# Optimization experiments

Measured on AMD Instinct MI355X. Metric: run time of the kernel, lower is better.

## Reference

```python
import jax, jax.numpy as jnp
import numpy as np

# Layered type graph: L layers of M nodes; layer 0 = basic types, layers >=1 reference earlier layers only.
L, M, D, P, S = 64, 2048, 128, 4, 2
NB = 11  # number of Kotlin basic types (kotlin.Any ... kotlin.Unit)
N = L * M


def setup_inputs() -> dict:
    key = jax.random.key(0)
    ks = jax.random.split(key, 8)
    rng = np.random.default_rng(0)
    basic_names = jnp.asarray(rng.integers(0, NB, size=(M,)), dtype=jnp.int32)
    # properties / superTypes point strictly to earlier layers (valid topological DAG)
    prop_ids = np.zeros((L, M, P), dtype=np.int32)
    super_ids = np.zeros((L, M, S), dtype=np.int32)
    for l in range(1, L):
        prop_ids[l] = rng.integers(0, l * M, size=(M, P))
        super_ids[l] = rng.integers(0, l * M, size=(M, S))
    prop_ids = jnp.asarray(prop_ids)
    super_ids = jnp.asarray(super_ids)
    sc = 0.05
    return {
        "basic_names": basic_names,
        "prop_ids": prop_ids,
        "super_ids": super_ids,
        "basic_table": jax.random.normal(ks[0], (NB, D), jnp.float32) * sc,
        "W_m": jax.random.normal(ks[1], (D, 4 * D), jnp.float32) * sc,
        "U_m": jax.random.normal(ks[2], (D, 4 * D), jnp.float32) * sc,
        "b_m": jnp.zeros((4 * D,), jnp.float32),
        "W_s": jax.random.normal(ks[3], (D, 4 * D), jnp.float32) * sc,
        "U_s": jax.random.normal(ks[4], (D, 4 * D), jnp.float32) * sc,
        "b_s": jnp.zeros((4 * D,), jnp.float32),
        "empty_members": jax.random.normal(ks[5], (D,), jnp.float32) * sc,
    }


def _lstm_last(seq, W, U, b):
    # seq: [T, B, D]; keras LSTM (tanh / sigmoid, gate order i,f,g,o); returns last hidden [B, D]
    T, B, Dh = seq.shape
    h = jnp.zeros((B, Dh), seq.dtype)
    c = jnp.zeros((B, Dh), seq.dtype)
    for t in range(T):  # T is a small static constant (P+1 or S+1)
        z = seq[t] @ W + h @ U + b  # [B, 4D]
        i, f, g, o = jnp.split(z, 4, axis=-1)
        c = jax.nn.sigmoid(f) * c + jax.nn.sigmoid(i) * jnp.tanh(g)
        h = jax.nn.sigmoid(o) * jnp.tanh(c)
    return h


def reference(basic_names, prop_ids, super_ids, basic_table, W_m, U_m, b_m, W_s, U_s, b_s, empty_members):
    emb = jnp.zeros((N, D), basic_table.dtype)
    emb = emb.at[:M].set(basic_table[basic_names])  # layer 0: basic type embedding lookup

    def step(emb, xs):
        l, pid, sid = xs  # pid:[M,P] sid:[M,S], all indices < l*M (already computed)
        prop_e = jnp.swapaxes(emb[pid], 0, 1)  # [P, M, D] irregular gather
        seq_m = jnp.concatenate([jnp.broadcast_to(empty_members, (1, M, D)), prop_e], axis=0)  # [P+1, M, D]
        h_m = _lstm_last(seq_m, W_m, U_m, b_m)  # embed_members
        sup_e = jnp.swapaxes(emb[sid], 0, 1)  # [S, M, D]
        seq_s = jnp.concatenate([sup_e, h_m[None]], axis=0)  # [S+1, M, D]
        h_s = _lstm_last(seq_s, W_s, U_s, b_s)  # embed_super_types
        emb = jax.lax.dynamic_update_slice(emb, h_s, (l * M, 0))
        return emb, None

    ls = jnp.arange(1, L, dtype=jnp.int32)
    emb, _ = jax.lax.scan(step, emb, (ls, prop_ids[1:], super_ids[1:]))
    return emb  # [N, D] == tf.convert_to_tensor(class_embeddings)
```

## Files before the change

### kernel.cpp

```cpp
#include <hip/hip_runtime.h>

typedef unsigned short u16;
typedef short s16x8 __attribute__((ext_vector_type(8)));
typedef float f32x4 __attribute__((ext_vector_type(4)));

#define LAYERS   64
#define M_NODES  2048
#define DIM      128
#define FD       512
#define CHUNK    16
#define NBLK     128
#define TPB      512
#define XPAD     136

__device__ __forceinline__ u16 f2bf(float f) {
    union { float f; unsigned int i; } v; v.f = f;
    unsigned int r = (v.i + 0x7FFFu + ((v.i >> 16) & 1u)) >> 16;
    return (u16)r;
}
__device__ __forceinline__ float sigm(float x) {
    return __builtin_amdgcn_rcpf(1.0f + __builtin_exp2f(-1.44269504f * x));
}
__device__ __forceinline__ float tanh_f(float x) {
    float ax = __builtin_fabsf(x);
    float t  = __builtin_exp2f(-2.88539008f * ax);
    float r  = (1.0f - t) * __builtin_amdgcn_rcpf(1.0f + t);
    return __builtin_copysignf(r, x);
}

__global__ void l0_kernel(const int* __restrict__ names, const float* __restrict__ table,
                          float* __restrict__ emb) {
    int v = blockIdx.x * blockDim.x + threadIdx.x;
    if (v >= M_NODES * (DIM / 4)) return;
    int row = v >> 5, c = v & 31;
    const float4* src = (const float4*)(table + (size_t)names[row] * DIM);
    ((float4*)(emb + (size_t)row * DIM))[c] = src[c];
}

__global__ void repack_kernel(const float* __restrict__ Wm, const float* __restrict__ Um,
                              const float* __restrict__ Ws, const float* __restrict__ Us,
                              u16* __restrict__ packed) {
    int t = blockIdx.x * blockDim.x + threadIdx.x;
    if (t >= 4 * 4 * 32 * 64) return;
    int lane = t & 63, ntg = (t >> 6) & 31, kc = (t >> 11) & 3, mat = t >> 13;
    const float* B = (mat == 0) ? Wm : (mat == 1) ? Um : (mat == 2) ? Ws : Us;
    int q = lane >> 4, nl = lane & 15;
    int kb = kc * 32 + q * 8;
    int n  = ntg * 16 + nl;
    u16* dst = packed + ((((size_t)mat * 4 + kc) * 32 + ntg) * 64 + lane) * 8;
    #pragma unroll
    for (int j = 0; j < 8; j++) dst[j] = f2bf(B[(size_t)(kb + j) * FD + n]);
}

template <bool PACKED>
__global__ __launch_bounds__(TPB, 2) void layer_kernel(
    float* __restrict__ emb, const int* __restrict__ prop_ids, const int* __restrict__ super_ids,
    const float* __restrict__ Wm, const float* __restrict__ Um, const float* __restrict__ bm,
    const float* __restrict__ Ws, const float* __restrict__ Us, const float* __restrict__ bs,
    const float* __restrict__ empty, const u16* __restrict__ packed, int l) {

    __shared__ __align__(16) u16  xs[6][CHUNK][XPAD];
    __shared__ __align__(16) u16  hbuf[2][CHUNK][XPAD];
    __shared__ __align__(16) u16  empty_s[XPAD];

    const int tid  = threadIdx.x;
    const int b    = blockIdx.x;
    const int g0   = b * CHUNK;
    const size_t row0 = (size_t)l * M_NODES + g0;

    const int wv   = tid >> 6;
    const int lane = tid & 63;
    const int q    = lane >> 4, nl = lane & 15;
    const int d    = wv * 16 + nl;

    if (tid < 384) {
        int quarter = tid & 3;
        int r    = tid >> 2;
        int slot = r >> 4;
        int node = r & 15;
        size_t idx;
        if (slot < 4) idx = (size_t)prop_ids [((size_t)l * M_NODES + g0 + node) * 4 + slot];
        else          idx = (size_t)super_ids[((size_t)l * M_NODES + g0 + node) * 2 + (slot - 4)];
        const float4* src = (const float4*)(emb + idx * DIM);
        u16* dst = &xs[slot][node][0];
        int e0 = quarter * 32;
        #pragma unroll
        for (int j = 0; j < 8; j++) {
            float4 v = src[(e0 >> 2) + j];
            int o = e0 + j * 4;
            dst[o] = f2bf(v.x); dst[o + 1] = f2bf(v.y);
            dst[o + 2] = f2bf(v.z); dst[o + 3] = f2bf(v.w);
        }
    } else if (tid < 384 + 128) {
        int dd = tid - 384;
        empty_s[dd] = f2bf(empty[dd]);
    }
    __syncthreads();

    auto load_bfrag_packed = [&](int mat, int kc, int g) -> s16x8 {
        return *(const s16x8*)(packed + ((((size_t)mat * 4 + kc) * 32 + (g * 8 + wv)) * 64 + lane) * 8);
    };
    auto load_bfrag_direct = [&](const float* B, int kc, int g) -> s16x8 {
        int kb = kc * 32 + q * 8;
        int n  = g * 128 + d;
        s16x8 f;
        #pragma unroll
        for (int j = 0; j < 8; j++) f[j] = (short)f2bf(B[(size_t)(kb + j) * FD + n]);
        return f;
    };
    auto load_afrag = [&](const u16* X , int kc) -> s16x8 {
        return *(const s16x8*)(X + (size_t)nl * XPAD + kc * 32 + q * 8);
    };

    auto run_phase = [&](const float* Wg, const float* Ug, const float* bias,
                         int matW, int matU, int nsteps, const int* slots,
                         bool write_hm, bool write_out) {
        s16x8 wf[4][4], uf[4][4];
        #pragma unroll
        for (int kc = 0; kc < 4; kc++) {
            #pragma unroll
            for (int g = 0; g < 4; g++) {
                if (PACKED) { wf[kc][g] = load_bfrag_packed(matW, kc, g);
                              uf[kc][g] = load_bfrag_packed(matU, kc, g); }
                else        { wf[kc][g] = load_bfrag_direct(Wg, kc, g);
                              uf[kc][g] = load_bfrag_direct(Ug, kc, g); }
            }
        }
        float bz[4];
        #pragma unroll
        for (int g = 0; g < 4; g++) bz[g] = bias[g * 128 + d];
        float cc[4] = {0.f, 0.f, 0.f, 0.f};

        #pragma unroll 1
        for (int t = 0; t < nsteps; t++) {
            int s = slots[t];
            f32x4 acc[4];
            #pragma unroll
            for (int g = 0; g < 4; g++) acc[g] = (f32x4){0.f, 0.f, 0.f, 0.f};
            #pragma unroll
            for (int kc = 0; kc < 4; kc++) {
                s16x8 a = (s < 0) ? *(const s16x8*)(&empty_s[kc * 32 + q * 8])
                                  : load_afrag(&xs[s][0][0], kc);
                #pragma unroll
                for (int g = 0; g < 4; g++)
                    acc[g] = __builtin_amdgcn_mfma_f32_16x16x32_bf16(a, wf[kc][g], acc[g], 0, 0, 0);
            }
            if (t > 0) {
                __syncthreads();
                const u16* hb = &hbuf[(t - 1) & 1][0][0];
                #pragma unroll
                for (int kc = 0; kc < 4; kc++) {
                    s16x8 a = load_afrag(hb, kc);
                    #pragma unroll
                    for (int g = 0; g < 4; g++)
                        acc[g] = __builtin_amdgcn_mfma_f32_16x16x32_bf16(a, uf[kc][g], acc[g], 0, 0, 0);
                }
            }
            bool last = (t == nsteps - 1);
            #pragma unroll
            for (int r2 = 0; r2 < 4; r2++) {
                int m = q * 4 + r2;
                float zi = acc[0][r2] + bz[0];
                float zf = acc[1][r2] + bz[1];
                float zg = acc[2][r2] + bz[2];
                float zo = acc[3][r2] + bz[3];
                float c  = sigm(zf) * cc[r2] + sigm(zi) * tanh_f(zg);
                cc[r2] = c;
                float h  = sigm(zo) * tanh_f(c);
                if (!last)          hbuf[t & 1][m][d] = f2bf(h);
                else if (write_hm)  xs[0][m][d] = f2bf(h);
                else if (write_out) emb[(row0 + m) * DIM + d] = h;
            }
        }
    };

    {
        const int slots_m[5] = {-1, 0, 1, 2, 3};
        run_phase(Wm, Um, bm, 0, 1, 5, slots_m, true, false);
    }
    {
        const int slots_s[3] = {4, 5, 0};
        run_phase(Ws, Us, bs, 2, 3, 3, slots_s, false, true);
    }
}

extern "C" void kernel_launch(void* const* d_in, const int* in_sizes, int n_in,
                              void* d_out, int out_size, void* d_ws, size_t ws_size,
                              hipStream_t stream) {
    const int*   names = (const int*)d_in[0];
    const int*   pids  = (const int*)d_in[1];
    const int*   sids  = (const int*)d_in[2];
    const float* table = (const float*)d_in[3];
    const float* Wm    = (const float*)d_in[4];
    const float* Um    = (const float*)d_in[5];
    const float* bm    = (const float*)d_in[6];
    const float* Ws    = (const float*)d_in[7];
    const float* Us    = (const float*)d_in[8];
    const float* bs    = (const float*)d_in[9];
    const float* empt  = (const float*)d_in[10];
    float* emb  = (float*)d_out;
    u16* packed = (u16*)d_ws;

    l0_kernel<<<256, 256, 0, stream>>>(names, table, emb);

    const size_t packed_bytes = (size_t)4 * 4 * 32 * 64 * 8 * sizeof(u16);
    if (ws_size >= packed_bytes) {
        repack_kernel<<<128, 256, 0, stream>>>(Wm, Um, Ws, Us, packed);
        for (int l = 1; l < LAYERS; l++)
            layer_kernel<true><<<NBLK, TPB, 0, stream>>>(emb, pids, sids, Wm, Um, bm,
                                                         Ws, Us, bs, empt, packed, l);
    } else {
        for (int l = 1; l < LAYERS; l++)
            layer_kernel<false><<<NBLK, TPB, 0, stream>>>(emb, pids, sids, Wm, Um, bm,
                                                          Ws, Us, bs, empt, packed, l);
    }
}
```

Before: 1.269 ms.

## Fuse all layers into one cooperative persistent kernel with grid sync

```diff
diff --git a/kernel.cpp b/kernel.cpp
--- a/kernel.cpp
+++ b/kernel.cpp
@@ -1,4 +1,7 @@
 #include <hip/hip_runtime.h>
+#include <hip/hip_cooperative_groups.h>
+
+namespace cg = cooperative_groups;
 
 typedef unsigned short u16;
 typedef short s16x8 __attribute__((ext_vector_type(8)));
@@ -53,6 +56,241 @@
 }
 
 template <bool PACKED>
+__global__ __launch_bounds__(TPB, 2) void fused_kernel(
+    float* __restrict__ emb, const int* __restrict__ prop_ids, const int* __restrict__ super_ids,
+    const float* __restrict__ Wm, const float* __restrict__ Um, const float* __restrict__ bm,
+    const float* __restrict__ Ws, const float* __restrict__ Us, const float* __restrict__ bs,
+    const float* __restrict__ empty, const u16* __restrict__ packed) {
+
+    cg::grid_group grid = cg::this_grid();
+
+    __shared__ __align__(16) u16  xs[6][CHUNK][XPAD];
+    __shared__ __align__(16) u16  hbuf[2][CHUNK][XPAD];
+    __shared__ float h1_s[DIM];
+
+    const int tid  = threadIdx.x;
+    const int b    = blockIdx.x;
+    const int g0   = b * CHUNK;
+    const int wv   = tid >> 6;
+    const int lane = tid & 63;
+    const int q    = lane >> 4, nl = lane & 15;
+    const int d    = wv * 16 + nl;
+
+    auto ldB = [&](const float* B, int mat, int kc, int g) -> s16x8 {
+        if (PACKED) {
+            return *(const s16x8*)(packed + ((((size_t)mat * 4 + kc) * 32 + (g * 8 + wv)) * 64 + lane) * 8);
+        } else {
+            int kb = kc * 32 + q * 8;
+            int n  = g * 128 + d;
+            s16x8 f;
+            #pragma unroll
+            for (int j = 0; j < 8; j++) f[j] = (short)f2bf(B[(size_t)(kb + j) * FD + n]);
+            return f;
+        }
+    };
+    auto load_afrag = [&](const u16* X , int kc) -> s16x8 {
+        return *(const s16x8*)(X + (size_t)nl * XPAD + kc * 32 + q * 8);
+    };
+
+    float bzm[4], bzs[4];
+    #pragma unroll
+    for (int g = 0; g < 4; g++) { bzm[g] = bm[g * 128 + d]; bzs[g] = bs[g * 128 + d]; }
+
+    float c1, h1;
+    {
+        float z0 = bzm[0], z1 = bzm[1], z2 = bzm[2], z3 = bzm[3];
+        for (int k = 0; k < DIM; k++) {
+            float e = empty[k];
+            const float* Wr = Wm + (size_t)k * FD + d;
+            z0 += e * Wr[0]; z1 += e * Wr[128]; z2 += e * Wr[256]; z3 += e * Wr[384];
+        }
+        (void)z1;
+        c1 = sigm(z0) * tanh_f(z2);
+        h1 = sigm(z3) * tanh_f(c1);
+        if (q == 0) h1_s[d] = h1;
+    }
+    __syncthreads();
+
+    float uh1[4];
+    {
+        s16x8 ha[4];
+        #pragma unroll
+        for (int kc = 0; kc < 4; kc++)
+            #pragma unroll
+            for (int j = 0; j < 8; j++) ha[kc][j] = (short)f2bf(h1_s[kc * 32 + q * 8 + j]);
+        f32x4 acc[4];
+        #pragma unroll
+        for (int g = 0; g < 4; g++) acc[g] = (f32x4){0.f, 0.f, 0.f, 0.f};
+        #pragma unroll
+        for (int kc = 0; kc < 4; kc++) {
+            #pragma unroll
+            for (int g = 0; g < 4; g++) {
+                s16x8 u = ldB(Um, 1, kc, g);
+                acc[g] = __builtin_amdgcn_mfma_f32_16x16x32_bf16(ha[kc], u, acc[g], 0, 0, 0);
+            }
+        }
+        #pragma unroll
+        for (int g = 0; g < 4; g++) uh1[g] = acc[g][0];
+    }
+
+    auto gates = [&](f32x4* acc, const float* bz, float* cc, int mode, int parity, int l) {
+        #pragma unroll
+        for (int r2 = 0; r2 < 4; r2++) {
+            int m = q * 4 + r2;
+            float zi = acc[0][r2] + bz[0];
+            float zf = acc[1][r2] + bz[1];
+            float zg = acc[2][r2] + bz[2];
+            float zo = acc[3][r2] + bz[3];
+            float c  = sigm(zf) * cc[r2] + sigm(zi) * tanh_f(zg);
+            cc[r2] = c;
+            float h  = sigm(zo) * tanh_f(c);
+            if (mode == 0)      hbuf[parity][m][d] = f2bf(h);
+            else if (mode == 1) xs[0][m][d] = f2bf(h);
+            else emb[((size_t)l * M_NODES + g0 + m) * DIM + d] = h;
+        }
+    };
+
+    for (int l = 1; l < LAYERS; l++) {
+        size_t gidx = 0; int quarter = 0, slot = 0, node = 0;
+        if (tid < 384) {
+            quarter = tid & 3;
+            int r = tid >> 2;
+            slot = r >> 4;
+            node = r & 15;
+            if (slot < 4) gidx = (size_t)prop_ids [((size_t)l * M_NODES + g0 + node) * 4 + slot];
+            else          gidx = (size_t)super_ids[((size_t)l * M_NODES + g0 + node) * 2 + (slot - 4)];
+        }
+        if (l > 1) { __threadfence(); grid.sync(); }
+
+        if (tid < 384) {
+            const float4* src = (const float4*)(emb + gidx * DIM);
+            u16* dst = &xs[slot][node][0];
+            int e0 = quarter * 32;
+            #pragma unroll
+            for (int j = 0; j < 8; j++) {
+                float4 v = src[(e0 >> 2) + j];
+                int o = e0 + j * 4;
+                dst[o] = f2bf(v.x); dst[o + 1] = f2bf(v.y);
+                dst[o + 2] = f2bf(v.z); dst[o + 3] = f2bf(v.w);
+            }
+        }
+        __syncthreads();
+
+        f32x4 zxm[4][4];
+        {
+            s16x8 wf[4][4];
+            #pragma unroll
+            for (int kc = 0; kc < 4; kc++)
+                #pragma unroll
+                for (int g = 0; g < 4; g++) wf[kc][g] = ldB(Wm, 0, kc, g);
+            #pragma unroll
+            for (int s = 0; s < 4; s++) {
+                #pragma unroll
+                for (int g = 0; g < 4; g++) zxm[s][g] = (f32x4){0.f, 0.f, 0.f, 0.f};
+                #pragma unroll
+                for (int kc = 0; kc < 4; kc++) {
+                    s16x8 a = load_afrag(&xs[s][0][0], kc);
+                    #pragma unroll
+                    for (int g = 0; g < 4; g++)
+                        zxm[s][g] = __builtin_amdgcn_mfma_f32_16x16x32_bf16(a, wf[kc][g], zxm[s][g], 0, 0, 0);
+                }
+            }
+        }
+
+        {
+            s16x8 uf[4][4];
+            #pragma unroll
+            for (int kc = 0; kc < 4; kc++)
+                #pragma unroll
+                for (int g = 0; g < 4; g++) uf[kc][g] = ldB(Um, 1, kc, g);
+            float cc[4] = {c1, c1, c1, c1};
+            {
+                f32x4 acc[4];
+                #pragma unroll
+                for (int g = 0; g < 4; g++) acc[g] = zxm[0][g] + uh1[g];
+                gates(acc, bzm, cc, 0, 1, l);
+            }
+            #pragma unroll
+            for (int t = 2; t <= 4; t++) {
+                __syncthreads();
+                const u16* hb = &hbuf[(t - 1) & 1][0][0];
+                f32x4 acc[4];
+                #pragma unroll
+                for (int g = 0; g < 4; g++) acc[g] = zxm[t - 1][g];
+                #pragma unroll
+                for (int kc = 0; kc < 4; kc++) {
+                    s16x8 a = load_afrag(hb, kc);
+                    #pragma unroll
+                    for (int g = 0; g < 4; g++)
+                        acc[g] = __builtin_amdgcn_mfma_f32_16x16x32_bf16(a, uf[kc][g], acc[g], 0, 0, 0);
+                }
+                if (t < 4) gates(acc, bzm, cc, 0, t & 1, l);
+                else       gates(acc, bzm, cc, 1, 0, l);
+            }
+        }
+
+        {
+            s16x8 uf[4][4], wf[4][4];
+            #pragma unroll
+            for (int kc = 0; kc < 4; kc++)
+                #pragma unroll
+                for (int g = 0; g < 4; g++) {
+                    uf[kc][g] = ldB(Us, 3, kc, g);
+                    wf[kc][g] = ldB(Ws, 2, kc, g);
+                }
+            f32x4 acc0[4], zxs1[4];
+            #pragma unroll
+            for (int g = 0; g < 4; g++) { acc0[g] = (f32x4){0.f,0.f,0.f,0.f}; zxs1[g] = (f32x4){0.f,0.f,0.f,0.f}; }
+            #pragma unroll
+            for (int kc = 0; kc < 4; kc++) {
+                s16x8 a4 = load_afrag(&xs[4][0][0], kc);
+                s16x8 a5 = load_afrag(&xs[5][0][0], kc);
+                #pragma unroll
+                for (int g = 0; g < 4; g++) {
+                    acc0[g] = __builtin_amdgcn_mfma_f32_16x16x32_bf16(a4, wf[kc][g], acc0[g], 0, 0, 0);
+                    zxs1[g] = __builtin_amdgcn_mfma_f32_16x16x32_bf16(a5, wf[kc][g], zxs1[g], 0, 0, 0);
+                }
+            }
+            float cc[4] = {0.f, 0.f, 0.f, 0.f};
+            gates(acc0, bzs, cc, 0, 0, l);
+            {
+                __syncthreads();
+                const u16* hb = &hbuf[0][0][0];
+                f32x4 acc[4];
+                #pragma unroll
+                for (int g = 0; g < 4; g++) acc[g] = zxs1[g];
+                #pragma unroll
+                for (int kc = 0; kc < 4; kc++) {
+                    s16x8 a = load_afrag(hb, kc);
+                    #pragma unroll
+                    for (int g = 0; g < 4; g++)
+                        acc[g] = __builtin_amdgcn_mfma_f32_16x16x32_bf16(a, uf[kc][g], acc[g], 0, 0, 0);
+                }
+                gates(acc, bzs, cc, 0, 1, l);
+            }
+            {
+                __syncthreads();
+                const u16* hb = &hbuf[1][0][0];
+                f32x4 acc[4];
+                #pragma unroll
+                for (int g = 0; g < 4; g++) acc[g] = (f32x4){0.f, 0.f, 0.f, 0.f};
+                #pragma unroll
+                for (int kc = 0; kc < 4; kc++) {
+                    s16x8 a  = load_afrag(&xs[0][0][0], kc);
+                    s16x8 ah = load_afrag(hb, kc);
+                    #pragma unroll
+                    for (int g = 0; g < 4; g++) {
+                        acc[g] = __builtin_amdgcn_mfma_f32_16x16x32_bf16(a,  wf[kc][g], acc[g], 0, 0, 0);
+                        acc[g] = __builtin_amdgcn_mfma_f32_16x16x32_bf16(ah, uf[kc][g], acc[g], 0, 0, 0);
+                    }
+                }
+                gates(acc, bzs, cc, 2, 0, l);
+            }
+        }
+    }
+}
+
+template <bool PACKED>
 __global__ __launch_bounds__(TPB, 2) void layer_kernel(
     float* __restrict__ emb, const int* __restrict__ prop_ids, const int* __restrict__ super_ids,
     const float* __restrict__ Wm, const float* __restrict__ Um, const float* __restrict__ bm,
@@ -108,7 +346,7 @@
         for (int j = 0; j < 8; j++) f[j] = (short)f2bf(B[(size_t)(kb + j) * FD + n]);
         return f;
     };
-    auto load_afrag = [&](const u16* X , int kc) -> s16x8 {
+    auto load_afrag = [&](const u16* X, int kc) -> s16x8 {
         return *(const s16x8*)(X + (size_t)nl * XPAD + kc * 32 + q * 8);
     };
 
@@ -204,14 +442,25 @@
     l0_kernel<<<256, 256, 0, stream>>>(names, table, emb);
 
     const size_t packed_bytes = (size_t)4 * 4 * 32 * 64 * 8 * sizeof(u16);
-    if (ws_size >= packed_bytes) {
+    const bool packed_ok = ws_size >= packed_bytes;
+    if (packed_ok)
         repack_kernel<<<128, 256, 0, stream>>>(Wm, Um, Ws, Us, packed);
-        for (int l = 1; l < LAYERS; l++)
-            layer_kernel<true><<<NBLK, TPB, 0, stream>>>(emb, pids, sids, Wm, Um, bm,
-                                                         Ws, Us, bs, empt, packed, l);
-    } else {
-        for (int l = 1; l < LAYERS; l++)
-            layer_kernel<false><<<NBLK, TPB, 0, stream>>>(emb, pids, sids, Wm, Um, bm,
-                                                          Ws, Us, bs, empt, packed, l);
-    }
-}
+
+    void* args[] = {(void*)&emb, (void*)&pids, (void*)&sids, (void*)&Wm, (void*)&Um, (void*)&bm,
+                    (void*)&Ws, (void*)&Us, (void*)&bs, (void*)&empt, (void*)&packed};
+    void (*kptr)(float*, const int*, const int*, const float*, const float*, const float*,
+                 const float*, const float*, const float*, const float*, const u16*) =
+        packed_ok ? fused_kernel<true> : fused_kernel<false>;
+    hipError_t err = hipLaunchCooperativeKernel((const void*)kptr, dim3(NBLK), dim3(TPB),
+                                                args, 0, stream);
+    if (err != hipSuccess) {
+        for (int l = 1; l < LAYERS; l++) {
+            if (packed_ok)
+                layer_kernel<true><<<NBLK, TPB, 0, stream>>>(emb, pids, sids, Wm, Um, bm,
+                                                             Ws, Us, bs, empt, packed, l);
+            else
+                layer_kernel<false><<<NBLK, TPB, 0, stream>>>(emb, pids, sids, Wm, Um, bm,
+                                                              Ws, Us, bs, empt, packed, l);
+        }
+    }
+}
```

New measurement: 3.731 ms. 2.94x slower.
